# Kernel optimization log

Measured on AMD Instinct MI355X. Metric: run time of the kernel, lower is better.

The kernel has to match this reference:

```python
import jax, jax.numpy as jnp
import numpy as np

B, T, D, H = 64, 2048, 128, 256
EPS = 1e-5


def setup_inputs() -> dict:
    key = jax.random.key(0)
    ks = jax.random.split(key, 20)
    s_d = 1.0 / np.sqrt(D)
    s_h = 1.0 / np.sqrt(H)
    s_2h = 1.0 / np.sqrt(2 * H)
    u = lambda k, shape, s: jax.random.uniform(k, shape, jnp.float32, -s, s)
    return {
        "x": jax.random.normal(ks[0], (B, T, D), jnp.float32),
        # gate input projections, stored (in, out)
        "Wi": u(ks[1], (D, H), s_d), "bi": u(ks[2], (H,), s_d),
        "Wf": u(ks[3], (D, H), s_d), "bf": u(ks[4], (H,), s_d),
        "Wc": u(ks[5], (D, H), s_d), "bc": u(ks[6], (H,), s_d),
        "Wo": u(ks[7], (D, H), s_d), "bo": u(ks[8], (H,), s_d),
        # recurrent projections (no bias)
        "Ui": u(ks[9], (H, H), s_h), "Uf": u(ks[10], (H, H), s_h),
        "Uc": u(ks[11], (H, H), s_h), "Uo": u(ks[12], (H, H), s_h),
        # KAN MLP: H -> 2H -> H
        "K1": u(ks[13], (H, 2 * H), s_h), "kb1": u(ks[14], (2 * H,), s_h),
        "K2": u(ks[15], (2 * H, H), s_2h), "kb2": u(ks[16], (H,), s_2h),
        # LayerNorm
        "gamma": jnp.ones((H,), jnp.float32), "beta": jnp.zeros((H,), jnp.float32),
    }


def _layernorm(h, gamma, beta):
    mu = jnp.mean(h, axis=-1, keepdims=True)
    var = jnp.mean(jnp.square(h - mu), axis=-1, keepdims=True)
    return (h - mu) * jax.lax.rsqrt(var + EPS) * gamma + beta


def _forward(x, Wi, bi, Wf, bf, Wc, bc, Wo, bo, Ui, Uf, Uc, Uo, K1, kb1, K2, kb2, gamma, beta):
    # Precompute input projections for all timesteps: (B,T,H) -> scan over T
    xi = jnp.einsum("btd,dh->bth", x, Wi) + bi
    xf = jnp.einsum("btd,dh->bth", x, Wf) + bf
    xc = jnp.einsum("btd,dh->bth", x, Wc) + bc
    xo = jnp.einsum("btd,dh->bth", x, Wo) + bo
    xs = jnp.stack([xi, xf, xc, xo], axis=0).transpose(2, 0, 1, 3)  # (T,4,B,H)

    h0 = jnp.zeros((x.shape[0], Wi.shape[1]), x.dtype)
    c0 = jnp.zeros_like(h0)

    def step(carry, xt):
        h, c = carry
        xi_t, xf_t, xc_t, xo_t = xt[0], xt[1], xt[2], xt[3]
        i_t = jax.nn.sigmoid(xi_t + h @ Ui)
        f_t = jax.nn.sigmoid(xf_t + h @ Uf)
        c_tilde = jnp.tanh(xc_t + h @ Uc)
        o_t = jax.nn.sigmoid(xo_t + h @ Uo)
        c = f_t * c + i_t * c_tilde
        c_tr = jnp.tanh(c @ K1 + kb1) @ K2 + kb2  # KAN transform
        h = o_t * jnp.tanh(c_tr)
        h = _layernorm(h, gamma, beta)  # dropout is identity in eval mode
        return (h, c), h

    (h, c), ys = jax.lax.scan(step, (h0, c0), xs)
    output = ys.transpose(1, 0, 2)  # (B,T,H)
    return output, h, c


def reference(x, Wi, bi, Wf, bf, Wc, bc, Wo, bo, Ui, Uf, Uc, Uo, K1, kb1, K2, kb2, gamma, beta):
    return _forward(x, Wi, bi, Wf, bf, Wc, bc, Wo, bo, Ui, Uf, Uc, Uo, K1, kb1, K2, kb2, gamma, beta)
```

## Files before the change

### kernel.cpp

```cpp
#include <hip/hip_runtime.h>

#define B 64
#define T 2048
#define D 128
#define H 256
#define H2 512
#define NP 4
#define CHUNK 8

#define ROW_U64 1536
#define WS_NEEDED ((size_t)B * ROW_U64 * 8)
#define SPIN_LIM (1 << 20)

__device__ __forceinline__ float sigmoid_f(float x) { return 1.f / (1.f + __expf(-x)); }
__device__ __forceinline__ float tanh_f(float x) {
    float e = __expf(2.f * x);
    return 1.f - 2.f / (e + 1.f);
}
__device__ __forceinline__ unsigned long long pack_tag(float v, unsigned int tag) {
    return ((unsigned long long)tag << 32) | (unsigned long long)__float_as_uint(v);
}
__device__ __forceinline__ float poll_tagged(const unsigned long long* __restrict__ ptr,
                                             unsigned int tag, bool& alive) {
    unsigned long long v;
    if (alive) {
        int cnt = 0;
        do {
            v = __hip_atomic_load(ptr, __ATOMIC_RELAXED, __HIP_MEMORY_SCOPE_AGENT);
            if ((unsigned int)(v >> 32) == tag)
                return __uint_as_float((unsigned int)v);
        } while (++cnt < SPIN_LIM);
        alive = false;
    }
    v = __hip_atomic_load(ptr, __ATOMIC_RELAXED, __HIP_MEMORY_SCOPE_AGENT);
    return __uint_as_float((unsigned int)v);
}

#define FMA4(A_, S_, W_) \
    A_.x = fmaf(S_, W_.x, A_.x); A_.y = fmaf(S_, W_.y, A_.y); \
    A_.z = fmaf(S_, W_.z, A_.z); A_.w = fmaf(S_, W_.w, A_.w);

__global__ __launch_bounds__(512) void scan_kernel(
    const float* __restrict__ x,
    const float* __restrict__ Wi, const float* __restrict__ bi,
    const float* __restrict__ Wf, const float* __restrict__ bf,
    const float* __restrict__ Wc, const float* __restrict__ bc,
    const float* __restrict__ Wo, const float* __restrict__ bo,
    const float* __restrict__ Ui, const float* __restrict__ Uf,
    const float* __restrict__ Uc, const float* __restrict__ Uo,
    const float* __restrict__ K1, const float* __restrict__ kb1,
    const float* __restrict__ K2, const float* __restrict__ kb2,
    const float* __restrict__ gamma, const float* __restrict__ beta,
    float* __restrict__ out,
    unsigned long long* __restrict__ ws)
{
    const int bid = blockIdx.x;
    const int b   = bid >> 2;
    const int p   = bid & 3;
    const int tid = threadIdx.x;

    __shared__ float k2lds[128 * 256];
    __shared__ float xw[CHUNK][256];
    __shared__ float red[2048];
    __shared__ float hs[H], cs[H], os[H], us[H], ts[128];

    const int kq  = tid >> 6;
    const int grp = tid & 63;
    const int gG  = grp >> 4;
    const int jG  = (grp & 15) * 4;

    const float* Ug = (gG == 0) ? Ui : (gG == 1) ? Uf : (gG == 2) ? Uc : Uo;
    const float* Wg = (gG == 0) ? Wi : (gG == 1) ? Wf : (gG == 2) ? Wc : Wo;

    float4 uw[32];
    #pragma unroll
    for (int k = 0; k < 32; ++k)
        uw[k] = *(const float4*)(Ug + (size_t)(kq * 32 + k) * H + p * 64 + jG);

    const int c1  = tid >> 2;
    const int ks  = tid & 3;
    float4 k1w[16];
    #pragma unroll
    for (int i = 0; i < 16; ++i) {
        const int j = (i + ks * 2) & 15;
        float4 v;
        v.x = K1[(size_t)(ks * 64 + j * 4 + 0) * H2 + p * 128 + c1];
        v.y = K1[(size_t)(ks * 64 + j * 4 + 1) * H2 + p * 128 + c1];
        v.z = K1[(size_t)(ks * 64 + j * 4 + 2) * H2 + p * 128 + c1];
        v.w = K1[(size_t)(ks * 64 + j * 4 + 3) * H2 + p * 128 + c1];
        k1w[i] = v;
    }

    for (int idx = tid; idx < 128 * 64; idx += 512) {
        int k = idx >> 6, jg = (idx & 63) * 4;
        *(float4*)&k2lds[k * 256 + jg] = *(const float4*)(K2 + (size_t)(p * 128 + k) * H + jg);
    }

    float bcat = 0.f;
    const float kb1r = kb1[p * 128 + c1];
    const float kb2r = kb2[tid >> 1];
    float4 gam4, bet4;
    if (tid < 256) {
        const int g = tid >> 6, jj = tid & 63;
        const float* bp = (g == 0) ? bi : (g == 1) ? bf : (g == 2) ? bc : bo;
        bcat = bp[p * 64 + jj];
    }
    if (tid < 64) {
        gam4 = *(const float4*)(gamma + tid * 4);
        bet4 = *(const float4*)(beta + tid * 4);
    }

    if (tid < 256) hs[tid] = 0.f;
    float c_reg = 0.f;

    const float* xrow = x + (size_t)b * T * D;
    float* yb = out + (size_t)b * T * H;
    unsigned long long* rowp  = ws + (size_t)b * ROW_U64;
    unsigned long long* slotC = rowp;
    unsigned long long* slotO = rowp + 256;
    unsigned long long* slotH = rowp + 512;
    const int dqu = __builtin_amdgcn_readfirstlane(kq);

    bool alive = true;
    __syncthreads();

    for (int t = 0; t < T; ++t) {
        const int tt8 = t & (CHUNK - 1);
        const unsigned int seq = (unsigned int)(t + 1);

        if (tt8 == 0) {
            const float* Wp = Wg + p * 64 + jG;
            #pragma unroll
            for (int pass = 0; pass < 2; ++pass) {
                float4 acc[4];
                #pragma unroll
                for (int r = 0; r < 4; ++r) acc[r] = make_float4(0.f, 0.f, 0.f, 0.f);
                #pragma unroll 4
                for (int dd = 0; dd < 16; ++dd) {
                    const int d = dqu * 16 + dd;
                    float4 w = *(const float4*)(Wp + (size_t)d * H);
                    #pragma unroll
                    for (int r = 0; r < 4; ++r) {
                        float xv = xrow[(size_t)(t + pass * 4 + r) * D + d];
                        FMA4(acc[r], xv, w);
                    }
                }
                #pragma unroll
                for (int r = 0; r < 4; ++r) {
                    *(float4*)&red[kq * 256 + grp * 4] = acc[r];
                    __syncthreads();
                    if (tid < 256) {
                        float s = bcat;
                        #pragma unroll
                        for (int q = 0; q < 8; ++q) s += red[q * 256 + tid];
                        xw[pass * 4 + r][tid] = s;
                    }
                    __syncthreads();
                }
            }
        }

        {
            float4 a = make_float4(0.f, 0.f, 0.f, 0.f);
            #pragma unroll
            for (int k4 = 0; k4 < 8; ++k4) {
                float4 hv = *(const float4*)&hs[kq * 32 + k4 * 4];
                FMA4(a, hv.x, uw[k4 * 4 + 0]);
                FMA4(a, hv.y, uw[k4 * 4 + 1]);
                FMA4(a, hv.z, uw[k4 * 4 + 2]);
                FMA4(a, hv.w, uw[k4 * 4 + 3]);
            }
            *(float4*)&red[kq * 256 + grp * 4] = a;
        }
        __syncthreads();

        if (tid < 64) {
            const int j = tid;
            float si = xw[tt8][j],        sf = xw[tt8][64 + j],
                  sg = xw[tt8][128 + j],  so = xw[tt8][192 + j];
            #pragma unroll
            for (int q = 0; q < 8; ++q) {
                si += red[q * 256 + j];
                sf += red[q * 256 + 64 + j];
                sg += red[q * 256 + 128 + j];
                so += red[q * 256 + 192 + j];
            }
            float iv = sigmoid_f(si), fv = sigmoid_f(sf);
            float gv = tanh_f(sg),    ov = sigmoid_f(so);
            float c = fmaf(fv, c_reg, iv * gv);
            c_reg = c;
            cs[p * 64 + j] = c;
            os[p * 64 + j] = ov;
            __hip_atomic_store(slotC + p * 64 + j, pack_tag(c, seq),
                               __ATOMIC_RELAXED, __HIP_MEMORY_SCOPE_AGENT);
            __hip_atomic_store(slotO + p * 64 + j, pack_tag(ov, seq),
                               __ATOMIC_RELAXED, __HIP_MEMORY_SCOPE_AGENT);
        } else if (tid < 448) {
            const int idx = tid - 64;
            if (idx < 192) {
                const int q  = (p + 1 + (idx >> 6)) & 3;
                const int gj = q * 64 + (idx & 63);
                cs[gj] = poll_tagged(slotC + gj, seq, alive);
            } else {
                const int i2 = idx - 192;
                const int q  = (p + 1 + (i2 >> 6)) & 3;
                const int gj = q * 64 + (i2 & 63);
                os[gj] = poll_tagged(slotO + gj, seq, alive);
            }
        }
        __syncthreads();

        {
            float a = 0.f;
            #pragma unroll
            for (int i = 0; i < 16; ++i) {
                const int j = (i + ks * 2) & 15;
                float4 cv = *(const float4*)&cs[ks * 64 + j * 4];
                a += cv.x * k1w[i].x + cv.y * k1w[i].y
                   + cv.z * k1w[i].z + cv.w * k1w[i].w;
            }
            a += __shfl_xor(a, 1);
            a += __shfl_xor(a, 2);
            if (ks == 0) ts[c1] = tanh_f(a + kb1r);
        }
        __syncthreads();

        {
            const int col = tid >> 1, kh = tid & 1;
            const float* kp0 = &k2lds[(kh * 64) * 256 + col];
            float a = 0.f;
            #pragma unroll
            for (int i = 0; i < 16; ++i) {
                float4 tv = *(const float4*)&ts[kh * 64 + i * 4];
                const float* kp = kp0 + i * 1024;
                a = fmaf(tv.x, kp[0],    a);
                a = fmaf(tv.y, kp[256],  a);
                a = fmaf(tv.z, kp[512],  a);
                a = fmaf(tv.w, kp[768],  a);
            }
            a += __shfl_xor(a, 1);
            if (kh == 0) {
                __hip_atomic_store(slotH + p * 256 + col, pack_tag(a, seq),
                                   __ATOMIC_RELAXED, __HIP_MEMORY_SCOPE_AGENT);
                const unsigned long long* q1 = slotH + (((p + 1) & 3) << 8) + col;
                const unsigned long long* q2 = slotH + (((p + 2) & 3) << 8) + col;
                const unsigned long long* q3 = slotH + (((p + 3) & 3) << 8) + col;
                unsigned long long v1 = 0, v2 = 0, v3 = 0;
                bool d1 = false, d2 = false, d3 = false;
                int cnt = 0;
                const int lim = alive ? SPIN_LIM : 2;
                while (true) {
                    if (!d1) v1 = __hip_atomic_load(q1, __ATOMIC_RELAXED, __HIP_MEMORY_SCOPE_AGENT);
                    if (!d2) v2 = __hip_atomic_load(q2, __ATOMIC_RELAXED, __HIP_MEMORY_SCOPE_AGENT);
                    if (!d3) v3 = __hip_atomic_load(q3, __ATOMIC_RELAXED, __HIP_MEMORY_SCOPE_AGENT);
                    d1 = d1 | ((unsigned int)(v1 >> 32) == seq);
                    d2 = d2 | ((unsigned int)(v2 >> 32) == seq);
                    d3 = d3 | ((unsigned int)(v3 >> 32) == seq);
                    if (d1 & d2 & d3) break;
                    if (++cnt > lim) { alive = false; break; }
                }
                float hp = a + __uint_as_float((unsigned int)v1)
                             + __uint_as_float((unsigned int)v2)
                             + __uint_as_float((unsigned int)v3) + kb2r;
                us[col] = os[col] * tanh_f(hp);
            }
        }
        __syncthreads();

        if (tid < 64) {
            float4 u4 = *(const float4*)&us[tid * 4];
            float s1 = u4.x + u4.y + u4.z + u4.w;
            float s2 = u4.x * u4.x + u4.y * u4.y + u4.z * u4.z + u4.w * u4.w;
            #pragma unroll
            for (int off = 32; off > 0; off >>= 1) {
                s1 += __shfl_xor(s1, off);
                s2 += __shfl_xor(s2, off);
            }
            float mu   = s1 * (1.f / 256.f);
            float var  = fmaf(-mu, mu, s2 * (1.f / 256.f));
            float rstd = rsqrtf(var + 1e-5f);
            float4 hn;
            hn.x = (u4.x - mu) * rstd * gam4.x + bet4.x;
            hn.y = (u4.y - mu) * rstd * gam4.y + bet4.y;
            hn.z = (u4.z - mu) * rstd * gam4.z + bet4.z;
            hn.w = (u4.w - mu) * rstd * gam4.w + bet4.w;
            *(float4*)&hs[tid * 4] = hn;
            if ((tid >> 4) == p) {
                *(float4*)(yb + (size_t)t * H + tid * 4) = hn;
                if (t == T - 1) {
                    *(float4*)(out + (size_t)B * T * H + (size_t)b * H + tid * 4) = hn;
                    float4 c4 = *(const float4*)&cs[tid * 4];
                    *(float4*)(out + (size_t)B * T * H + (size_t)B * H + (size_t)b * H + tid * 4) = c4;
                }
            }
        }
        __syncthreads();
    }
}

extern "C" void kernel_launch(void* const* d_in, const int* in_sizes, int n_in,
                              void* d_out, int out_size, void* d_ws, size_t ws_size,
                              hipStream_t stream) {
    (void)in_sizes; (void)n_in; (void)out_size;
    if (ws_size < WS_NEEDED) return;

    const float* x     = (const float*)d_in[0];
    const float* Wi    = (const float*)d_in[1];
    const float* bi    = (const float*)d_in[2];
    const float* Wf    = (const float*)d_in[3];
    const float* bf    = (const float*)d_in[4];
    const float* Wc    = (const float*)d_in[5];
    const float* bc    = (const float*)d_in[6];
    const float* Wo    = (const float*)d_in[7];
    const float* bo    = (const float*)d_in[8];
    const float* Ui    = (const float*)d_in[9];
    const float* Uf    = (const float*)d_in[10];
    const float* Uc    = (const float*)d_in[11];
    const float* Uo    = (const float*)d_in[12];
    const float* K1    = (const float*)d_in[13];
    const float* kb1   = (const float*)d_in[14];
    const float* K2    = (const float*)d_in[15];
    const float* kb2   = (const float*)d_in[16];
    const float* gamma = (const float*)d_in[17];
    const float* beta  = (const float*)d_in[18];
    float* out = (float*)d_out;

    scan_kernel<<<dim3(B * NP), dim3(512), 0, stream>>>(
        x, Wi, bi, Wf, bf, Wc, bc, Wo, bo,
        Ui, Uf, Uc, Uo, K1, kb1, K2, kb2, gamma, beta, out,
        (unsigned long long*)d_ws);
}
```

Baseline: 15.30 ms.

## Overlap next-step input projection with cross-block spin and split K2 across registers/LDS

The per-chunk input projection burst, which needed eight barrier-separated reductions every eight steps, becomes a rolling prefetch. Each step computes the input projection for t+CHUNK after issuing its tagged hidden-state store and before spinning for peer partitions, so the wait on other blocks hides useful work. K2 is split so half the weights live in registers (32 floats per thread) and half in a smaller LDS array, with the cross-half reduction done by a wave shuffle at offset 32 rather than between adjacent lanes. This adds register pressure and one extra barrier per step, and changes which threads hold each output column.

New measurement: 25.71 ms. +68.0%, slower.

```diff
diff --git a/kernel.cpp b/kernel.cpp
--- a/kernel.cpp
+++ b/kernel.cpp
@@ -59,7 +59,7 @@
     const int p   = bid & 3;
     const int tid = threadIdx.x;
 
-    __shared__ float k2lds[128 * 256];
+    __shared__ float k2lds2[64 * 256];
     __shared__ float xw[CHUNK][256];
     __shared__ float red[2048];
     __shared__ float hs[H], cs[H], os[H], us[H], ts[128];
@@ -68,6 +68,9 @@
     const int grp = tid & 63;
     const int gG  = grp >> 4;
     const int jG  = (grp & 15) * 4;
+    const int col = kq * 32 + (grp & 31);
+    const int kh  = grp >> 5;
+    const int kh64 = kh * 64;
 
     const float* Ug = (gG == 0) ? Ui : (gG == 1) ? Uf : (gG == 2) ? Uc : Uo;
     const float* Wg = (gG == 0) ? Wi : (gG == 1) ? Wf : (gG == 2) ? Wc : Wo;
@@ -91,14 +94,21 @@
         k1w[i] = v;
     }
 
-    for (int idx = tid; idx < 128 * 64; idx += 512) {
+    float k2r[32];
+    #pragma unroll
+    for (int kk = 0; kk < 32; ++kk)
+        k2r[kk] = K2[(size_t)(p * 128 + kh64 + kk) * H + col];
+
+    for (int idx = tid; idx < 64 * 64; idx += 512) {
         int k = idx >> 6, jg = (idx & 63) * 4;
-        *(float4*)&k2lds[k * 256 + jg] = *(const float4*)(K2 + (size_t)(p * 128 + k) * H + jg);
+        int grow = (k >> 5) * 64 + 32 + (k & 31);
+        *(float4*)&k2lds2[k * 256 + jg] =
+            *(const float4*)(K2 + (size_t)(p * 128 + grow) * H + jg);
     }
 
     float bcat = 0.f;
     const float kb1r = kb1[p * 128 + c1];
-    const float kb2r = kb2[tid >> 1];
+    const float kb2r = kb2[col];
     float4 gam4, bet4;
     if (tid < 256) {
         const int g = tid >> 6, jj = tid & 63;
@@ -124,41 +134,31 @@
     bool alive = true;
     __syncthreads();
 
+    for (int r8 = 0; r8 < CHUNK; ++r8) {
+        float4 acc = make_float4(0.f, 0.f, 0.f, 0.f);
+        const float* Wp = Wg + p * 64 + jG;
+        #pragma unroll 4
+        for (int dd = 0; dd < 16; ++dd) {
+            const int d = dqu * 16 + dd;
+            float4 w = *(const float4*)(Wp + (size_t)d * H);
+            float xv = xrow[(size_t)r8 * D + d];
+            FMA4(acc, xv, w);
+        }
+        *(float4*)&red[kq * 256 + grp * 4] = acc;
+        __syncthreads();
+        if (tid < 256) {
+            float s = bcat;
+            #pragma unroll
+            for (int q = 0; q < 8; ++q) s += red[q * 256 + tid];
+            xw[r8][tid] = s;
+        }
+        __syncthreads();
+    }
+
     for (int t = 0; t < T; ++t) {
         const int tt8 = t & (CHUNK - 1);
         const unsigned int seq = (unsigned int)(t + 1);
-
-        if (tt8 == 0) {
-            const float* Wp = Wg + p * 64 + jG;
-            #pragma unroll
-            for (int pass = 0; pass < 2; ++pass) {
-                float4 acc[4];
-                #pragma unroll
-                for (int r = 0; r < 4; ++r) acc[r] = make_float4(0.f, 0.f, 0.f, 0.f);
-                #pragma unroll 4
-                for (int dd = 0; dd < 16; ++dd) {
-                    const int d = dqu * 16 + dd;
-                    float4 w = *(const float4*)(Wp + (size_t)d * H);
-                    #pragma unroll
-                    for (int r = 0; r < 4; ++r) {
-                        float xv = xrow[(size_t)(t + pass * 4 + r) * D + d];
-                        FMA4(acc[r], xv, w);
-                    }
-                }
-                #pragma unroll
-                for (int r = 0; r < 4; ++r) {
-                    *(float4*)&red[kq * 256 + grp * 4] = acc[r];
-                    __syncthreads();
-                    if (tid < 256) {
-                        float s = bcat;
-                        #pragma unroll
-                        for (int q = 0; q < 8; ++q) s += red[q * 256 + tid];
-                        xw[pass * 4 + r][tid] = s;
-                    }
-                    __syncthreads();
-                }
-            }
-        }
+        const int tx = t + CHUNK;
 
         {
             float4 a = make_float4(0.f, 0.f, 0.f, 0.f);
@@ -225,45 +225,73 @@
         }
         __syncthreads();
 
+        float k2part = 0.f;
         {
-            const int col = tid >> 1, kh = tid & 1;
-            const float* kp0 = &k2lds[(kh * 64) * 256 + col];
-            float a = 0.f;
-            #pragma unroll
-            for (int i = 0; i < 16; ++i) {
-                float4 tv = *(const float4*)&ts[kh * 64 + i * 4];
+            #pragma unroll
+            for (int i = 0; i < 8; ++i) {
+                float4 tv = *(const float4*)&ts[kh64 + i * 4];
+                k2part = fmaf(tv.x, k2r[i * 4 + 0], k2part);
+                k2part = fmaf(tv.y, k2r[i * 4 + 1], k2part);
+                k2part = fmaf(tv.z, k2r[i * 4 + 2], k2part);
+                k2part = fmaf(tv.w, k2r[i * 4 + 3], k2part);
+            }
+            const float* kp0 = &k2lds2[(kh * 32) * 256 + col];
+            #pragma unroll
+            for (int i = 0; i < 8; ++i) {
+                float4 tv = *(const float4*)&ts[kh64 + 32 + i * 4];
                 const float* kp = kp0 + i * 1024;
-                a = fmaf(tv.x, kp[0],    a);
-                a = fmaf(tv.y, kp[256],  a);
-                a = fmaf(tv.z, kp[512],  a);
-                a = fmaf(tv.w, kp[768],  a);
-            }
-            a += __shfl_xor(a, 1);
-            if (kh == 0) {
-                __hip_atomic_store(slotH + p * 256 + col, pack_tag(a, seq),
+                k2part = fmaf(tv.x, kp[0],   k2part);
+                k2part = fmaf(tv.y, kp[256], k2part);
+                k2part = fmaf(tv.z, kp[512], k2part);
+                k2part = fmaf(tv.w, kp[768], k2part);
+            }
+            k2part += __shfl_xor(k2part, 32);
+            if (kh == 0)
+                __hip_atomic_store(slotH + p * 256 + col, pack_tag(k2part, seq),
                                    __ATOMIC_RELAXED, __HIP_MEMORY_SCOPE_AGENT);
-                const unsigned long long* q1 = slotH + (((p + 1) & 3) << 8) + col;
-                const unsigned long long* q2 = slotH + (((p + 2) & 3) << 8) + col;
-                const unsigned long long* q3 = slotH + (((p + 3) & 3) << 8) + col;
-                unsigned long long v1 = 0, v2 = 0, v3 = 0;
-                bool d1 = false, d2 = false, d3 = false;
-                int cnt = 0;
-                const int lim = alive ? SPIN_LIM : 2;
-                while (true) {
-                    if (!d1) v1 = __hip_atomic_load(q1, __ATOMIC_RELAXED, __HIP_MEMORY_SCOPE_AGENT);
-                    if (!d2) v2 = __hip_atomic_load(q2, __ATOMIC_RELAXED, __HIP_MEMORY_SCOPE_AGENT);
-                    if (!d3) v3 = __hip_atomic_load(q3, __ATOMIC_RELAXED, __HIP_MEMORY_SCOPE_AGENT);
-                    d1 = d1 | ((unsigned int)(v1 >> 32) == seq);
-                    d2 = d2 | ((unsigned int)(v2 >> 32) == seq);
-                    d3 = d3 | ((unsigned int)(v3 >> 32) == seq);
-                    if (d1 & d2 & d3) break;
-                    if (++cnt > lim) { alive = false; break; }
+            if (tx < T) {
+                float4 acc = make_float4(0.f, 0.f, 0.f, 0.f);
+                const float* Wp = Wg + p * 64 + jG;
+                #pragma unroll 4
+                for (int dd = 0; dd < 16; ++dd) {
+                    const int d = dqu * 16 + dd;
+                    float4 w = *(const float4*)(Wp + (size_t)d * H);
+                    float xv = xrow[(size_t)tx * D + d];
+                    FMA4(acc, xv, w);
                 }
-                float hp = a + __uint_as_float((unsigned int)v1)
-                             + __uint_as_float((unsigned int)v2)
-                             + __uint_as_float((unsigned int)v3) + kb2r;
-                us[col] = os[col] * tanh_f(hp);
-            }
+                *(float4*)&red[kq * 256 + grp * 4] = acc;
+            }
+        }
+        __syncthreads();
+
+        if (tx < T && tid < 256) {
+            float s = bcat;
+            #pragma unroll
+            for (int q = 0; q < 8; ++q) s += red[q * 256 + tid];
+            xw[tt8][tid] = s;
+        }
+        if (kh == 0) {
+            const unsigned long long* q1 = slotH + (((p + 1) & 3) << 8) + col;
+            const unsigned long long* q2 = slotH + (((p + 2) & 3) << 8) + col;
+            const unsigned long long* q3 = slotH + (((p + 3) & 3) << 8) + col;
+            unsigned long long v1 = 0, v2 = 0, v3 = 0;
+            bool d1 = false, d2 = false, d3 = false;
+            int cnt = 0;
+            const int lim = alive ? SPIN_LIM : 2;
+            while (true) {
+                if (!d1) v1 = __hip_atomic_load(q1, __ATOMIC_RELAXED, __HIP_MEMORY_SCOPE_AGENT);
+                if (!d2) v2 = __hip_atomic_load(q2, __ATOMIC_RELAXED, __HIP_MEMORY_SCOPE_AGENT);
+                if (!d3) v3 = __hip_atomic_load(q3, __ATOMIC_RELAXED, __HIP_MEMORY_SCOPE_AGENT);
+                d1 = d1 | ((unsigned int)(v1 >> 32) == seq);
+                d2 = d2 | ((unsigned int)(v2 >> 32) == seq);
+                d3 = d3 | ((unsigned int)(v3 >> 32) == seq);
+                if (d1 & d2 & d3) break;
+                if (++cnt > lim) { alive = false; break; }
+            }
+            float hp = k2part + __uint_as_float((unsigned int)v1)
+                              + __uint_as_float((unsigned int)v2)
+                              + __uint_as_float((unsigned int)v3) + kb2r;
+            us[col] = os[col] * tanh_f(hp);
         }
         __syncthreads();
 
```
